# Optimization experiments

Hardware: AMD Instinct MI355X
Metric: run time of the kernel (lower is better)

The kernel has to match this reference:

```python
import jax, jax.numpy as jnp
import numpy as np


def conv(x, w, b):
    # NCHW input, OIHW kernel, stride 1, SAME padding (matches pad=k//2 in torch)
    y = jax.lax.conv_general_dilated(x, w, (1, 1), 'SAME',
                                     dimension_numbers=('NCHW', 'OIHW', 'NCHW'))
    return y + b[None, :, None, None]


def maxpool2(x):
    return jax.lax.reduce_window(x, -jnp.inf, jax.lax.max, (1, 1, 2, 2), (1, 1, 2, 2), 'VALID')


def up(x, s):
    n, c, h, w = x.shape
    # PyTorch nn.Upsample(bilinear, align_corners=False) == half-pixel bilinear
    return jax.image.resize(x, (n, c, h * s, w * s), 'bilinear')


def lin_scan(a, u, axis):
    # h_t = a_t * h_{t-1} + (1 - a_t) * u_t, h_{-1} = 0, via parallel associative scan
    def comb(p, q):
        a1, b1 = p
        a2, b2 = q
        return a1 * a2, a2 * b1 + b2
    return jax.lax.associative_scan(comb, (a, (1.0 - a) * u), axis=axis)[1]


_W_SPECS = [('w_s1', (3, 3, 3, 3)), ('w_mc', (16, 12, 3, 3)), ('w2', (16, 3, 5, 5)),
            ('w3', (32, 16, 3, 3)), ('w4', (32, 32, 3, 3)), ('w5', (32, 32, 3, 3)),
            ('w6', (64, 32, 3, 3)), ('w6s', (64, 64, 3, 3)), ('w7', (32, 96, 3, 3)),
            ('w8', (16, 64, 3, 3)), ('w9', (64, 32, 3, 3)), ('w10', (64, 16, 3, 3)),
            ('w11', (3, 64, 3, 3))]


def setup_inputs():
    key = jax.random.key(0)
    ks = jax.random.split(key, 32)
    inp = {'x': jax.random.normal(ks[0], (2, 3, 512, 512), jnp.float32)}
    for i, (name, sh) in enumerate(_W_SPECS):
        inp[name] = jax.random.normal(ks[i + 1], sh, jnp.float32) * 0.1
        inp['b' + name[1:]] = jax.random.normal(ks[i + 16], (sh[0],), jnp.float32) * 0.01
    return inp


def _forward(x, w_s1, b_s1, w_mc, b_mc, w2, b2, w3, b3, w4, b4, w5, b5, w6, b6,
             w6s, b6s, w7, b7, w8, b8, w9, b9, w10, b10, w11, b11):
    relu = jax.nn.relu
    # multiscale feature input for the spatial RNN
    s1 = conv(x, w_s1, b_s1)
    s2 = maxpool2(s1)
    s3 = maxpool2(s2)
    s4 = maxpool2(s3)
    multi = jnp.concatenate([s1, up(s2, 2), up(s3, 4), up(s4, 8)], axis=1)  # [N,12,H,W]
    ms = conv(multi, w_mc, b_mc)  # [N,16,H,W]
    # gate-prediction encoder/decoder
    c2 = relu(conv(x, w2, b2))                 # [N,16,H,W]
    c3 = relu(conv(maxpool2(c2), w3, b3))      # [N,32,H/2]
    c4 = relu(conv(maxpool2(c3), w4, b4))      # [N,32,H/4]
    c5 = relu(conv(maxpool2(c4), w5, b5))      # [N,32,H/8]
    c6 = relu(conv(maxpool2(c5), w6, b6))      # [N,64,H/16]
    c6re = up(relu(conv(up(c6, 2), w6s, b6s)), 2)               # [N,64,H/4]
    c7 = up(relu(conv(jnp.concatenate([c6re, c4], 1), w7, b7)), 2)  # [N,32,H/2]
    c8 = up(relu(conv(jnp.concatenate([c7, c3], 1), w8, b8)), 2)    # [N,16,H]
    c9 = jnp.tanh(conv(jnp.concatenate([c8, c2], 1), w9, b9))       # [N,64,H,W]
    gx1, gy1, gx2, gy2 = c9[:, 0:16], c9[:, 16:32], c9[:, 32:48], c9[:, 48:64]
    # source quirk: vertical first-pass loops gate with gx1 for steps i>=1 but gy1 row-0 at init
    gate_v = jnp.concatenate([gy1[:, :, 0:1, :], gx1[:, :, 1:, :]], axis=2)
    # first pass: 4-directional gated linear scans over the multiscale features
    h1 = lin_scan(gx1, ms, axis=3)                     # left->right
    h2 = lin_scan(gx1, ms[:, :, :, ::-1], axis=3)      # right->left (stored in scan order)
    h3 = lin_scan(gate_v, ms, axis=2)                  # top->bottom
    h4 = lin_scan(gate_v, ms[:, :, ::-1, :], axis=2)   # bottom->top (stored in scan order)
    # second pass
    h5 = lin_scan(gx2, h1, axis=3)
    h6 = lin_scan(gx2, h2[:, :, :, ::-1], axis=3)
    h7 = lin_scan(gy2, h3, axis=2)
    h8 = lin_scan(gy2, h4[:, :, ::-1, :], axis=2)
    elt_max = jnp.maximum(jnp.maximum(h5, h6), jnp.maximum(h7, h8))
    c10 = relu(conv(elt_max, w10, b10))
    return relu(conv(c10, w11, b11))


def reference(x, w_s1, b_s1, w_mc, b_mc, w2, b2, w3, b3, w4, b4, w5, b5, w6, b6,
              w6s, b6s, w7, b7, w8, b8, w9, b9, w10, b10, w11, b11):
    return _forward(x, w_s1, b_s1, w_mc, b_mc, w2, b2, w3, b3, w4, b4, w5, b5,
                    w6, b6, w6s, b6s, w7, b7, w8, b8, w9, b9, w10, b10, w11, b11)
```

## Files before the change

### kernel.cpp

```cpp
#include <hip/hip_runtime.h>
#include <math.h>

typedef float  f32x4  __attribute__((ext_vector_type(4)));
typedef short  bf16x8 __attribute__((ext_vector_type(8)));

__device__ __forceinline__ ushort f2bf(float f) {
    unsigned u = __float_as_uint(f);
    unsigned r = (u + 0x7fffu + ((u >> 16) & 1u)) >> 16;
    return (ushort)r;
}
__device__ __forceinline__ float bf2f(ushort u) {
    return __uint_as_float(((unsigned)u) << 16);
}
__device__ __forceinline__ float fast_tanh(float x) {
    float e = __expf(2.f * x);
    return 1.f - 2.f / (e + 1.f);
}

__global__ __launch_bounds__(256) void packw_k(
    const float* __restrict__ w, ushort* __restrict__ dst,
    int OCpad, int OCreal, int Cin, int nkb)
{
    int i = blockIdx.x * 256 + threadIdx.x;
    int total = nkb * 9 * OCpad * 32;
    if (i >= total) return;
    int ic32 = i & 31;
    int oc = (i >> 5) % OCpad;
    int t  = (i / (32 * OCpad)) % 9;
    int kb = i / (32 * OCpad * 9);
    int gic = kb * 32 + ic32;
    float v = 0.f;
    if (oc < OCreal && gic < Cin) v = w[((size_t)oc * Cin + gic) * 9 + t];
    dst[i] = f2bf(v);
}

template<int OCB, int NKB, int ACT, int OUTMODE>
__global__ __launch_bounds__(256, 3) void gconv_k(
    const ushort* __restrict__ s0, int n0,
    const ushort* __restrict__ s1, int n1,
    const ushort* __restrict__ Wp, const float* __restrict__ bias,
    void* __restrict__ outp, int H, int W)
{
    constexpr int NB = OCB / 16;
    const int n  = blockIdx.z;
    const int x0 = blockIdx.x * 16, y0 = blockIdx.y * 8;
    const int tid = threadIdx.x;
    const int wid = tid >> 6, lane = tid & 63;
    const int lm = lane & 15, kg = lane >> 4, k0 = kg * 8;
    const bool edge = (x0 == 0) || (x0 + 16 >= W) || (y0 == 0) || (y0 + 8 >= H);
    const int ntot = n0 + n1;
    const size_t HW = (size_t)H * W;

    const ushort* bptr[NKB];
    int bstr[NKB];
    bool bpad[NKB];
#pragma unroll
    for (int kb = 0; kb < NKB; kb++) {
        int gch = kb * 32 + k0;
        if (gch < n0)        { bptr[kb] = s0 + HW * (size_t)(n * n0) + gch;        bstr[kb] = n0; bpad[kb] = false; }
        else if (gch < ntot) { bptr[kb] = s1 + HW * (size_t)(n * n1) + (gch - n0); bstr[kb] = n1; bpad[kb] = false; }
        else                 { bptr[kb] = s0; bstr[kb] = 0; bpad[kb] = true; }
    }

    f32x4 acc[2][NB];
#pragma unroll
    for (int a = 0; a < 2; a++)
#pragma unroll
        for (int b = 0; b < NB; b++) acc[a][b] = (f32x4){0.f, 0.f, 0.f, 0.f};

#pragma unroll
    for (int kb = 0; kb < NKB; kb++) {
        bf16x8 areg[2][9];
#pragma unroll
        for (int ky = 0; ky < 3; ky++)
#pragma unroll
        for (int kx = 0; kx < 3; kx++) {
            const int t = ky * 3 + kx;
#pragma unroll
            for (int mt = 0; mt < 2; mt++) {
                int row = y0 + 2 * wid + mt + ky - 1;
                int xl  = x0 + lm + kx - 1;
                bf16x8 z = (bf16x8){0,0,0,0,0,0,0,0};
                if (!bpad[kb] && (!edge || (row >= 0 && row < H && xl >= 0 && xl < W)))
                    z = *(const bf16x8*)&bptr[kb][((size_t)(row * W + xl)) * bstr[kb]];
                areg[mt][t] = z;
            }
        }
#pragma unroll
        for (int t = 0; t < 9; t++) {
            bf16x8 wf[NB];
#pragma unroll
            for (int nb = 0; nb < NB; nb++)
                wf[nb] = *(const bf16x8*)&Wp[(((kb * 9) + t) * OCB + nb * 16 + lm) * 32 + k0];
#pragma unroll
            for (int nb = 0; nb < NB; nb++) {
#pragma unroll
                for (int mt = 0; mt < 2; mt++)
                    acc[mt][nb] = __builtin_amdgcn_mfma_f32_16x16x32_bf16(areg[mt][t], wf[nb], acc[mt][nb], 0, 0, 0);
            }
        }
    }

    if constexpr (OUTMODE == 0) {
        float* outf = (float*)outp;
#pragma unroll
        for (int mt = 0; mt < 2; mt++) {
            int y = y0 + 2 * wid + mt;
            int x = x0 + kg * 4;
#pragma unroll
            for (int nb = 0; nb < NB; nb++) {
                int oc = nb * 16 + lm;
                float bv = bias[oc];
                float r0 = acc[mt][nb][0] + bv, r1 = acc[mt][nb][1] + bv;
                float r2 = acc[mt][nb][2] + bv, r3 = acc[mt][nb][3] + bv;
                if (ACT == 1) { r0=fmaxf(r0,0.f); r1=fmaxf(r1,0.f); r2=fmaxf(r2,0.f); r3=fmaxf(r3,0.f); }
                if (ACT == 2) { r0=fast_tanh(r0); r1=fast_tanh(r1); r2=fast_tanh(r2); r3=fast_tanh(r3); }
                float4 o; o.x=r0; o.y=r1; o.z=r2; o.w=r3;
                *(float4*)&outf[(((size_t)n * OCB + oc) * H + y) * W + x] = o;
            }
        }
    } else {
        ushort* outb = (ushort*)outp;
        __shared__ ushort Ls[8 * 16 * OCB];
#pragma unroll
        for (int mt = 0; mt < 2; mt++) {
            int yy = 2 * wid + mt;
#pragma unroll
            for (int nb = 0; nb < NB; nb++) {
                int oc = nb * 16 + lm;
                float bv = bias[oc];
#pragma unroll
                for (int r = 0; r < 4; r++) {
                    float v = acc[mt][nb][r] + bv;
                    if (ACT == 1) v = fmaxf(v, 0.f);
                    if (ACT == 2) v = fast_tanh(v);
                    Ls[(yy * 16 + kg * 4 + r) * OCB + oc] = f2bf(v);
                }
            }
        }
        __syncthreads();
#pragma unroll
        for (int q = 0; q < NB; q++) {
            int off = tid * (NB * 8) + q * 8;
            int p = off / OCB, wv = off % OCB;
            int yy = p >> 4, xx = p & 15;
            *(bf16x8*)&outb[((size_t)((n * H + y0 + yy)) * W + x0 + xx) * OCB + wv] =
                *(const bf16x8*)&Ls[off];
        }
    }
}

__global__ __launch_bounds__(256, 3) void gconv11_k(
    const ushort* __restrict__ A, const ushort* __restrict__ Wp,
    const float* __restrict__ bias, float* __restrict__ out)
{
    const int n  = blockIdx.z;
    const int x0 = blockIdx.x * 16, y0 = blockIdx.y * 8;
    const int tid = threadIdx.x;
    const int wid = tid >> 6, lane = tid & 63;
    const int lm = lane & 15, kg = lane >> 4, k0 = kg * 8;
    const bool edge = (x0 == 0) || (x0 == 496) || (y0 == 0) || (y0 == 504);
    const size_t nbase = (size_t)n * 262144 * 64;

    f32x4 acc[2];
    acc[0] = (f32x4){0.f,0.f,0.f,0.f};
    acc[1] = (f32x4){0.f,0.f,0.f,0.f};

#pragma unroll
    for (int kb = 0; kb < 2; kb++) {
        bf16x8 areg[2][9];
#pragma unroll
        for (int ky = 0; ky < 3; ky++)
#pragma unroll
        for (int kx = 0; kx < 3; kx++) {
            const int t = ky * 3 + kx;
#pragma unroll
            for (int mt = 0; mt < 2; mt++) {
                int row = y0 + 2 * wid + mt + ky - 1;
                int xl  = x0 + lm + kx - 1;
                bf16x8 z = (bf16x8){0,0,0,0,0,0,0,0};
                if (!edge || (row >= 0 && row < 512 && xl >= 0 && xl < 512))
                    z = *(const bf16x8*)&A[nbase + ((size_t)(row * 512 + xl)) * 64 + kb * 32 + k0];
                areg[mt][t] = z;
            }
        }
#pragma unroll
        for (int t = 0; t < 9; t++) {
            bf16x8 bfr = *(const bf16x8*)&Wp[((kb * 9 + t) * 16 + lm) * 32 + k0];
#pragma unroll
            for (int mt = 0; mt < 2; mt++)
                acc[mt] = __builtin_amdgcn_mfma_f32_16x16x32_bf16(areg[mt][t], bfr, acc[mt], 0, 0, 0);
        }
    }

    if (lm < 3) {
        float bv = bias[lm];
#pragma unroll
        for (int mt = 0; mt < 2; mt++) {
            int y = y0 + 2 * wid + mt;
            int x = x0 + kg * 4;
            float4 o;
            o.x = fmaxf(acc[mt][0] + bv, 0.f);
            o.y = fmaxf(acc[mt][1] + bv, 0.f);
            o.z = fmaxf(acc[mt][2] + bv, 0.f);
            o.w = fmaxf(acc[mt][3] + bv, 0.f);
            *(float4*)&out[(((size_t)n * 3 + lm) * 512 + y) * 512 + x] = o;
        }
    }
}

__global__ __launch_bounds__(256) void pool_nhwc_k(
    const ushort* __restrict__ in, ushort* __restrict__ out, int C8, int Ho, int Wo)
{
    int idx = blockIdx.x * 256 + threadIdx.x;
    int total = 2 * Ho * Wo * C8;
    if (idx >= total) return;
    int s = idx % C8; int pix = idx / C8;
    int x = pix % Wo; int t = pix / Wo; int y = t % Ho; int n = t / Ho;
    int C = C8 * 8;
    const ushort* p = in + ((size_t)((n * 2 * Ho + 2 * y) * (2 * Wo) + 2 * x)) * C + s * 8;
    bf16x8 a = *(const bf16x8*)p;
    bf16x8 b = *(const bf16x8*)(p + C);
    bf16x8 c = *(const bf16x8*)(p + (size_t)(2 * Wo) * C);
    bf16x8 d = *(const bf16x8*)(p + (size_t)(2 * Wo) * C + C);
    ushort r[8];
#pragma unroll
    for (int j = 0; j < 8; j++) {
        float m = fmaxf(fmaxf(bf2f((ushort)a[j]), bf2f((ushort)b[j])),
                        fmaxf(bf2f((ushort)c[j]), bf2f((ushort)d[j])));
        r[j] = f2bf(m);
    }
    *(bf16x8*)&out[(size_t)pix * C + s * 8] = *(bf16x8*)r;
}

__global__ __launch_bounds__(256) void up_nhwc_k(
    const ushort* __restrict__ in, ushort* __restrict__ out, int C8, int Hi, int Wi)
{
    int Ho = Hi * 2, Wo = Wi * 2;
    int idx = blockIdx.x * 256 + threadIdx.x;
    int total = 2 * Ho * Wo * C8;
    if (idx >= total) return;
    int s = idx % C8; int pix = idx / C8;
    int x = pix % Wo; int t = pix / Wo; int y = t % Ho; int n = t / Ho;
    int C = C8 * 8;
    float sx = (x + 0.5f) * 0.5f - 0.5f;
    float sy = (y + 0.5f) * 0.5f - 0.5f;
    int ix0 = (int)floorf(sx), iy0 = (int)floorf(sy);
    float fx = sx - ix0, fy = sy - iy0;
    int ix1 = ix0 + 1, iy1 = iy0 + 1;
    ix0 = ix0 < 0 ? 0 : ix0;           iy0 = iy0 < 0 ? 0 : iy0;
    ix1 = ix1 > Wi - 1 ? Wi - 1 : ix1; iy1 = iy1 > Hi - 1 ? Hi - 1 : iy1;
    const ushort* base = in + (size_t)n * Hi * Wi * C + s * 8;
    bf16x8 v00 = *(const bf16x8*)&base[((size_t)iy0 * Wi + ix0) * C];
    bf16x8 v01 = *(const bf16x8*)&base[((size_t)iy0 * Wi + ix1) * C];
    bf16x8 v10 = *(const bf16x8*)&base[((size_t)iy1 * Wi + ix0) * C];
    bf16x8 v11 = *(const bf16x8*)&base[((size_t)iy1 * Wi + ix1) * C];
    ushort r[8];
#pragma unroll
    for (int j = 0; j < 8; j++) {
        float a = bf2f((ushort)v00[j]), b = bf2f((ushort)v01[j]);
        float c = bf2f((ushort)v10[j]), d = bf2f((ushort)v11[j]);
        float top = a + fx * (b - a);
        float bot = c + fx * (d - c);
        r[j] = f2bf(top + fy * (bot - top));
    }
    *(bf16x8*)&out[(size_t)pix * C + s * 8] = *(bf16x8*)r;
}

__global__ __launch_bounds__(256) void cvt16_k(
    const float* __restrict__ src, ushort* __restrict__ dst)
{
    int idx = blockIdx.x * 256 + threadIdx.x;
    int x = idx & 511, y = (idx >> 9) & 511, n = idx >> 18;
    const float* base = src + (size_t)n * 16 * 262144 + y * 512 + x;
    ushort vals[16];
#pragma unroll
    for (int c = 0; c < 16; c++) vals[c] = f2bf(base[(size_t)c * 262144]);
    ushort* d = dst + (size_t)idx * 16;
    *(bf16x8*)(d)     = *(bf16x8*)(vals);
    *(bf16x8*)(d + 8) = *(bf16x8*)(vals + 8);
}

template<int K, int OCB, int ACT, int PIX, int OUTW>
__global__ __launch_bounds__(256, 3) void conv_k(
    const float* __restrict__ src0, int c0,
    const float* __restrict__ src1, int c1,
    const float* __restrict__ src2, int c2,
    const float* __restrict__ src3, int c3,
    const float* __restrict__ w, const float* __restrict__ bias,
    void* __restrict__ outp, int H, int W, int OC, int ocChunks)
{
    constexpr int TW = 32, TH = 8 * PIX, P = K / 2;
    constexpr int TLW = TW + K - 1, TLH = TH + K - 1;
    constexpr int TLWP = (K == 3) ? 36 : 40;
    constexpr int CB = 4;
    __shared__ float tile[CB][TLH][TLWP];

    const int z   = blockIdx.z;
    const int n   = z / ocChunks;
    const int ocb = (z - n * ocChunks) * OCB;
    const int tx  = threadIdx.x & 31;
    const int ty  = threadIdx.x >> 5;
    const int x0  = blockIdx.x * TW, y0 = blockIdx.y * TH;
    const int Cin = c0 + c1 + c2 + c3;

    float acc[OCB][PIX];
#pragma unroll
    for (int i = 0; i < OCB; i++)
#pragma unroll
        for (int p = 0; p < PIX; p++) acc[i][p] = 0.f;

    int cgbase = 0;
#pragma unroll
    for (int s = 0; s < 4; s++) {
        const float* sp = (s == 0) ? src0 : (s == 1) ? src1 : (s == 2) ? src2 : src3;
        const int    cn = (s == 0) ? c0   : (s == 1) ? c1   : (s == 2) ? c2   : c3;
        for (int cb = 0; cb < cn; cb += CB) {
            const int nch = (cn - cb < CB) ? (cn - cb) : CB;
            __syncthreads();
            for (int idx = threadIdx.x; idx < nch * TLH * TLW; idx += 256) {
                int ch = idx / (TLH * TLW); int rem = idx - ch * (TLH * TLW);
                int r = rem / TLW, cc = rem - r * TLW;
                int gy = y0 + r - P, gx = x0 + cc - P;
                float vv = 0.f;
                if (gy >= 0 && gy < H && gx >= 0 && gx < W)
                    vv = sp[(size_t)(n * cn + cb + ch) * H * W + (size_t)gy * W + gx];
                tile[ch][r][cc] = vv;
            }
            __syncthreads();
            for (int c = 0; c < nch; c++) {
                float v[PIX + K - 1][K];
#pragma unroll
                for (int r = 0; r < PIX + K - 1; r++)
#pragma unroll
                    for (int cc = 0; cc < K; cc++)
                        v[r][cc] = tile[c][ty * PIX + r][tx + cc];
                const float* wc = w + ((size_t)ocb * Cin + (cgbase + cb + c)) * (K * K);
#pragma unroll
                for (int oc = 0; oc < OCB; oc++) {
                    const float* wo = wc + (size_t)oc * Cin * (K * K);
#pragma unroll
                    for (int ky = 0; ky < K; ky++)
#pragma unroll
                        for (int kx = 0; kx < K; kx++) {
                            float ww = wo[ky * K + kx];
#pragma unroll
                            for (int p = 0; p < PIX; p++)
                                acc[oc][p] = fmaf(ww, v[ky + p][kx], acc[oc][p]);
                        }
                }
            }
        }
        cgbase += cn;
    }

    const int xx = x0 + tx, yy = y0 + ty * PIX;
    if constexpr (OUTW == 0) {
        float* out = (float*)outp;
#pragma unroll
        for (int oc = 0; oc < OCB; oc++) {
            int o = ocb + oc;
            float b = bias[o];
#pragma unroll
            for (int p = 0; p < PIX; p++) {
                float r = acc[oc][p] + b;
                if (ACT == 1) r = fmaxf(r, 0.f);
                if (ACT == 2) r = tanhf(r);
                out[(((size_t)n * OC + o) * H + (yy + p)) * W + xx] = r;
            }
        }
    } else {
        ushort* ob = (ushort*)outp;
#pragma unroll
        for (int p = 0; p < PIX; p++) {
            ushort v16[16];
#pragma unroll
            for (int oc = 0; oc < OCB; oc++) {
                float r = acc[oc][p] + bias[oc];
                if (ACT == 1) r = fmaxf(r, 0.f);
                if (ACT == 2) r = tanhf(r);
                v16[oc] = f2bf(r);
            }
            ushort* d = &ob[(((size_t)n * H + (yy + p)) * W + xx) * 16];
            *(bf16x8*)d       = *(bf16x8*)v16;
            *(bf16x8*)(d + 8) = *(bf16x8*)(v16 + 8);
        }
    }
}

__global__ __launch_bounds__(256) void pool_k(
    const float* __restrict__ in, float* __restrict__ out, int NC, int H, int W)
{
    int H2 = H >> 1, W2 = W >> 1;
    int total = NC * H2 * W2;
    int idx = blockIdx.x * 256 + threadIdx.x;
    if (idx >= total) return;
    int x = idx % W2; int t = idx / W2; int y = t % H2; int q = t / H2;
    const float* p = in + ((size_t)q * H + 2 * y) * W + 2 * x;
    out[idx] = fmaxf(fmaxf(p[0], p[1]), fmaxf(p[W], p[W + 1]));
}

__global__ __launch_bounds__(256) void up_k(
    const float* __restrict__ in, float* __restrict__ out, int NC, int Hi, int Wi, int s)
{
    int Ho = Hi * s, Wo = Wi * s;
    int total = NC * Ho * Wo;
    int idx = blockIdx.x * 256 + threadIdx.x;
    if (idx >= total) return;
    int x = idx % Wo; int t = idx / Wo; int y = t % Ho; int q = t / Ho;
    float inv = 1.0f / (float)s;
    float sx = (x + 0.5f) * inv - 0.5f;
    float sy = (y + 0.5f) * inv - 0.5f;
    int ix0 = (int)floorf(sx), iy0 = (int)floorf(sy);
    float fx = sx - ix0, fy = sy - iy0;
    int ix1 = ix0 + 1, iy1 = iy0 + 1;
    ix0 = ix0 < 0 ? 0 : ix0;           iy0 = iy0 < 0 ? 0 : iy0;
    ix1 = ix1 > Wi - 1 ? Wi - 1 : ix1; iy1 = iy1 > Hi - 1 ? Hi - 1 : iy1;
    const float* p = in + (size_t)q * Hi * Wi;
    float v00 = p[(size_t)iy0 * Wi + ix0], v01 = p[(size_t)iy0 * Wi + ix1];
    float v10 = p[(size_t)iy1 * Wi + ix0], v11 = p[(size_t)iy1 * Wi + ix1];
    float top = v00 + fx * (v01 - v00);
    float bot = v10 + fx * (v11 - v10);
    out[idx] = top + fy * (bot - top);
}

__device__ __forceinline__ void scan_pair(const float a[8], float x1[8], float x2[8], int lane)
{
    float P = 1.f, Q1 = 0.f, Q2 = 0.f;
#pragma unroll
    for (int j = 0; j < 8; j++) {
        float av = a[j];
        Q1 = fmaf(av, Q1, (1.f - av) * x1[j]);
        Q2 = fmaf(av, Q2, (1.f - av) * x2[j]);
        P *= av;
    }
#pragma unroll
    for (int d = 1; d < 64; d <<= 1) {
        float Pp  = __shfl_up(P,  (unsigned)d);
        float Q1p = __shfl_up(Q1, (unsigned)d);
        float Q2p = __shfl_up(Q2, (unsigned)d);
        if (lane >= d) {
            Q1 = fmaf(P, Q1p, Q1);
            Q2 = fmaf(P, Q2p, Q2);
            P *= Pp;
        }
    }
    float h1in = __shfl_up(Q1, 1u);
    float h2in = __shfl_up(Q2, 1u);
    if (lane == 0) { h1in = 0.f; h2in = 0.f; }
    float s1 = h1in, s2 = h2in;
#pragma unroll
    for (int j = 0; j < 8; j++) {
        float av = a[j];
        s1 = fmaf(av, s1, (1.f - av) * x1[j]);
        s2 = fmaf(av, s2, (1.f - av) * x2[j]);
        x1[j] = s1; x2[j] = s2;
    }
}

__global__ __launch_bounds__(256) void scan_h_fused(
    const float* __restrict__ c9, const float* __restrict__ ms,
    float* __restrict__ hm)
{
    int gw   = (blockIdx.x * 256 + threadIdx.x) >> 6;
    int lane = threadIdx.x & 63;
    int y = gw & 511; int nc = gw >> 9; int c = nc & 15; int n = nc >> 4;
    const float* a1row = c9 + ((((size_t)n * 64 + c)      * 512 + y) << 9);
    const float* a2row = c9 + ((((size_t)n * 64 + 32 + c) * 512 + y) << 9);
    const size_t rowoff = (size_t)gw << 9;
    const float* ur = ms + rowoff;
    int t0 = lane << 3;

    float a1[8], a2[8], x1[8], x2[8];
    {
        float4 b0 = *(const float4*)(a1row + t0);
        float4 b1 = *(const float4*)(a1row + t0 + 4);
        a1[0]=b0.x; a1[1]=b0.y; a1[2]=b0.z; a1[3]=b0.w;
        a1[4]=b1.x; a1[5]=b1.y; a1[6]=b1.z; a1[7]=b1.w;
    }
    {
        float4 b0 = *(const float4*)(a2row + t0);
        float4 b1 = *(const float4*)(a2row + t0 + 4);
        a2[0]=b0.x; a2[1]=b0.y; a2[2]=b0.z; a2[3]=b0.w;
        a2[4]=b1.x; a2[5]=b1.y; a2[6]=b1.z; a2[7]=b1.w;
    }
    {
        float4 b0 = *(const float4*)(ur + t0);
        float4 b1 = *(const float4*)(ur + t0 + 4);
        x1[0]=b0.x; x1[1]=b0.y; x1[2]=b0.z; x1[3]=b0.w;
        x1[4]=b1.x; x1[5]=b1.y; x1[6]=b1.z; x1[7]=b1.w;
    }
    {
        float4 r0 = *(const float4*)(ur + (508 - t0));
        float4 r1 = *(const float4*)(ur + (504 - t0));
        x2[0]=r0.w; x2[1]=r0.z; x2[2]=r0.y; x2[3]=r0.x;
        x2[4]=r1.w; x2[5]=r1.z; x2[6]=r1.y; x2[7]=r1.x;
    }

    scan_pair(a1, x1, x2, lane);

    float r[8];
#pragma unroll
    for (int j = 0; j < 8; j++) r[j] = __shfl(x2[7 - j], 63 - lane);

    scan_pair(a2, x1, r, lane);

    float w0[4], w1[4];
#pragma unroll
    for (int j = 0; j < 4; j++) { w0[j] = fmaxf(x1[j], r[j]); w1[j] = fmaxf(x1[j+4], r[j+4]); }
    *(float4*)(hm + rowoff + t0)     = make_float4(w0[0], w0[1], w0[2], w0[3]);
    *(float4*)(hm + rowoff + t0 + 4) = make_float4(w1[0], w1[1], w1[2], w1[3]);
}

#define SV_DECODE \
    int g = blockIdx.x * 256 + threadIdx.x; \
    int x = g & 511; int nc = (g >> 9) & 31; int seg = g >> 14; \
    int c = nc & 15; int n = nc >> 4; int ys = seg << 6; (void)c; (void)n;

__global__ __launch_bounds__(256) void sv_a(
    const float* __restrict__ c9, const float* __restrict__ ms, float* __restrict__ SB)
{
    SV_DECODE
    const float* gx1 = c9 + (((size_t)n * 64 + c)      << 18) + x;
    const float* gy1 = c9 + (((size_t)n * 64 + 16 + c) << 18) + x;
    const float* u   = ms + ((size_t)nc << 18) + x;
    float P = 1.f, Q3 = 0.f, Q4 = 0.f;
    for (int i = 0; i < 64; i++) {
        int y = ys + i;
        float g3 = (y == 0) ? gy1[0] : gx1[(size_t)y << 9];
        float uf = u[(size_t)y << 9];
        float ub = u[(size_t)(511 - y) << 9];
        Q3 = fmaf(g3, Q3, (1.f - g3) * uf);
        Q4 = fmaf(g3, Q4, (1.f - g3) * ub);
        P *= g3;
    }
    SB[g] = P; SB[131072 + g] = Q3; SB[262144 + g] = Q4;
}

__global__ __launch_bounds__(256) void sv_b(
    float* __restrict__ c9, const float* __restrict__ ms,
    float* __restrict__ SB, float* __restrict__ h3buf)
{
    SV_DECODE
    const float* gx1 = c9 + (((size_t)n * 64 + c)      << 18) + x;
    const float* gy1 = c9 + (((size_t)n * 64 + 16 + c) << 18) + x;
    const float* gy2 = c9 + (((size_t)n * 64 + 48 + c) << 18) + x;
    float*       h4p = c9 + (((size_t)n * 64 + 32 + c) << 18) + x;
    const float* u   = ms + ((size_t)nc << 18) + x;
    float*       h3p = h3buf + ((size_t)nc << 18) + x;
    int gc = g & 16383;
    float s3 = 0.f, s4 = 0.f;
    for (int j = 0; j < seg; j++) {
        float Pj  = SB[j * 16384 + gc];
        float Q3j = SB[131072 + j * 16384 + gc];
        float Q4j = SB[262144 + j * 16384 + gc];
        s3 = fmaf(Pj, s3, Q3j);
        s4 = fmaf(Pj, s4, Q4j);
    }
    float P7 = 1.f, Q7 = 0.f;
    for (int i = 0; i < 64; i++) {
        int y = ys + i;
        float g3 = (y == 0) ? gy1[0] : gx1[(size_t)y << 9];
        float uf = u[(size_t)y << 9];
        float ub = u[(size_t)(511 - y) << 9];
        s3 = fmaf(g3, s3, (1.f - g3) * uf);
        s4 = fmaf(g3, s4, (1.f - g3) * ub);
        h3p[(size_t)y << 9] = s3;
        h4p[(size_t)y << 9] = s4;
        float g7 = gy2[(size_t)y << 9];
        Q7 = fmaf(g7, Q7, (1.f - g7) * s3);
        P7 *= g7;
    }
    SB[393216 + g] = P7; SB[524288 + g] = Q7;
}

__global__ __launch_bounds__(256) void sv_c(
    const float* __restrict__ c9, const float* __restrict__ h3buf,
    float* __restrict__ SB, float* __restrict__ hm)
{
    SV_DECODE
    const float* gy2 = c9 + (((size_t)n * 64 + 48 + c) << 18) + x;
    const float* h4p = c9 + (((size_t)n * 64 + 32 + c) << 18) + x;
    const float* h3p = h3buf + ((size_t)nc << 18) + x;
    float*       o   = hm + ((size_t)nc << 18) + x;
    int gc = g & 16383;
    float s7 = 0.f;
    for (int j = 0; j < seg; j++) {
        float Pj = SB[393216 + j * 16384 + gc];
        float Qj = SB[524288 + j * 16384 + gc];
        s7 = fmaf(Pj, s7, Qj);
    }
    float P8 = 1.f, Q8 = 0.f;
    for (int i = 0; i < 64; i++) {
        int y = ys + i;
        float g7 = gy2[(size_t)y << 9];
        float hv = h3p[(size_t)y << 9];
        s7 = fmaf(g7, s7, (1.f - g7) * hv);
        o[(size_t)y << 9] = fmaxf(o[(size_t)y << 9], s7);
        float u8 = h4p[(size_t)(511 - y) << 9];
        Q8 = fmaf(g7, Q8, (1.f - g7) * u8);
        P8 *= g7;
    }
    SB[655360 + g] = P8; SB[786432 + g] = Q8;
}

__global__ __launch_bounds__(256) void sv_d(
    const float* __restrict__ c9, const float* __restrict__ SB, float* __restrict__ hm)
{
    SV_DECODE
    const float* gy2 = c9 + (((size_t)n * 64 + 48 + c) << 18) + x;
    const float* h4p = c9 + (((size_t)n * 64 + 32 + c) << 18) + x;
    float*       o   = hm + ((size_t)nc << 18) + x;
    int gc = g & 16383;
    float s8 = 0.f;
    for (int j = 0; j < seg; j++) {
        float Pj = SB[655360 + j * 16384 + gc];
        float Qj = SB[786432 + j * 16384 + gc];
        s8 = fmaf(Pj, s8, Qj);
    }
    for (int i = 0; i < 64; i++) {
        int y = ys + i;
        float g7 = gy2[(size_t)y << 9];
        float u8 = h4p[(size_t)(511 - y) << 9];
        s8 = fmaf(g7, s8, (1.f - g7) * u8);
        o[(size_t)y << 9] = fmaxf(o[(size_t)y << 9], s8);
    }
}

extern "C" void kernel_launch(void* const* d_in, const int* in_sizes, int n_in,
                              void* d_out, int out_size, void* d_ws, size_t ws_size,
                              hipStream_t stream)
{
    const float* x    = (const float*)d_in[0];
    const float* w_s1 = (const float*)d_in[1];  const float* b_s1 = (const float*)d_in[2];
    const float* w_mc = (const float*)d_in[3];  const float* b_mc = (const float*)d_in[4];
    const float* w2   = (const float*)d_in[5];  const float* b2   = (const float*)d_in[6];
    const float* w3   = (const float*)d_in[7];  const float* b3   = (const float*)d_in[8];
    const float* w4   = (const float*)d_in[9];  const float* b4   = (const float*)d_in[10];
    const float* w5   = (const float*)d_in[11]; const float* b5   = (const float*)d_in[12];
    const float* w6   = (const float*)d_in[13]; const float* b6   = (const float*)d_in[14];
    const float* w6s  = (const float*)d_in[15]; const float* b6s  = (const float*)d_in[16];
    const float* w7   = (const float*)d_in[17]; const float* b7   = (const float*)d_in[18];
    const float* w8   = (const float*)d_in[19]; const float* b8   = (const float*)d_in[20];
    const float* w9   = (const float*)d_in[21]; const float* b9   = (const float*)d_in[22];
    const float* w10  = (const float*)d_in[23]; const float* b10  = (const float*)d_in[24];
    const float* w11  = (const float*)d_in[25]; const float* b11  = (const float*)d_in[26];
    float* out = (float*)d_out;
    float* ws  = (float*)d_ws;

    const size_t NEEDED = 60817408ull * 4ull;
    if (ws_size < NEEDED) return;

    float* MS    = ws;
    float* C9    = ws + 8388608;
    float* H3REG = ws + 41943040;
    float* AR    = ws + 50331648;

    ushort* WREG = (ushort*)AR;
    ushort* wp3  = WREG + 0;      ushort* wp4  = WREG + 9216;
    ushort* wp5  = WREG + 18432;  ushort* wp6  = WREG + 27648;
    ushort* wp6s = WREG + 46080;  ushort* wp7  = WREG + 82944;
    ushort* wp8  = WREG + 110592; ushort* wp9  = WREG + 119808;
    ushort* wp10 = WREG + 138240; ushort* wp11 = WREG + 156672;

    ushort* C2b = (ushort*)(AR + 163840);
    float* s1f = AR + 4358144;
    float* s2f = AR + 5931008;
    float* s3f = AR + 6324224;
    float* s4f = AR + 6422528;
    float* u2  = H3REG + 0;
    float* u3  = H3REG + 1572864;
    float* u4  = H3REG + 3145728;
    ushort* p2    = (ushort*)(AR + 4358144);
    ushort* c3    = (ushort*)(AR + 5406720);
    ushort* p3    = (ushort*)(AR + 7503872);
    ushort* c4    = (ushort*)(AR + 8028160);
    ushort* p4    = (ushort*)(AR + 8552448);
    ushort* c5    = (ushort*)(AR + 8683520);
    ushort* p5    = (ushort*)(AR + 8814592);
    ushort* c6    = (ushort*)(AR + 8847360);
    ushort* u6    = (ushort*)(AR + 8912896);
    ushort* t6    = (ushort*)(AR + 9175040);
    ushort* c6re  = (ushort*)(AR + 9437184);
    ushort* c7pre = (ushort*)(AR + 7503872);
    ushort* c7    = (ushort*)(AR + 8028160);
    ushort* c8pre = (ushort*)(AR + 4358144);
    ushort* c8b   = (ushort*)(AR + 5406720);
    float* SB  = AR + 163840;
    float* HM  = AR + 1081344;
    float* H3  = H3REG;
    ushort* A10 = (ushort*)H3REG;
    ushort* A11 = (ushort*)C9;

    auto cdiv = [](int a, int b) { return (a + b - 1) / b; };

    packw_k<<<36,256,0,stream>>>(w3,  wp3,  32, 32, 16, 1);
    packw_k<<<36,256,0,stream>>>(w4,  wp4,  32, 32, 32, 1);
    packw_k<<<36,256,0,stream>>>(w5,  wp5,  32, 32, 32, 1);
    packw_k<<<72,256,0,stream>>>(w6,  wp6,  64, 64, 32, 1);
    packw_k<<<144,256,0,stream>>>(w6s, wp6s, 64, 64, 64, 2);
    packw_k<<<108,256,0,stream>>>(w7,  wp7,  32, 32, 96, 3);
    packw_k<<<36,256,0,stream>>>(w8,  wp8,  16, 16, 64, 2);
    packw_k<<<72,256,0,stream>>>(w9,  wp9,  64, 64, 32, 1);
    packw_k<<<72,256,0,stream>>>(w10, wp10, 64, 64, 16, 1);
    packw_k<<<36,256,0,stream>>>(w11, wp11, 16, 3,  64, 2);

    conv_k<5,16,1,2,1><<<dim3(16,32,2),256,0,stream>>>(x,3,nullptr,0,nullptr,0,nullptr,0,
                                                       w2,b2, C2b, 512,512,16,1);
    conv_k<3,3,0,2,0><<<dim3(16,32,2),256,0,stream>>>(x,3,nullptr,0,nullptr,0,nullptr,0,
                                                      w_s1,b_s1, s1f, 512,512,3,1);
    pool_k<<<cdiv(2*3*256*256,256),256,0,stream>>>(s1f, s2f, 6, 512, 512);
    pool_k<<<cdiv(2*3*128*128,256),256,0,stream>>>(s2f, s3f, 6, 256, 256);
    pool_k<<<cdiv(2*3*64*64,  256),256,0,stream>>>(s3f, s4f, 6, 128, 128);
    up_k<<<6144,256,0,stream>>>(s2f, u2, 6, 256, 256, 2);
    up_k<<<6144,256,0,stream>>>(s3f, u3, 6, 128, 128, 4);
    up_k<<<6144,256,0,stream>>>(s4f, u4, 6, 64, 64, 8);
    conv_k<3,16,0,2,0><<<dim3(16,32,2),256,0,stream>>>(s1f,3,u2,3,u3,3,u4,3,
                                                       w_mc,b_mc, MS, 512,512,16,1);

    pool_nhwc_k<<<1024,256,0,stream>>>(C2b, p2, 2, 256, 256);
    gconv_k<32,1,1,1><<<dim3(16,32,2),256,0,stream>>>(p2,16,nullptr,0, wp3,b3, c3, 256,256);
    pool_nhwc_k<<<512,256,0,stream>>>(c3, p3, 4, 128, 128);
    gconv_k<32,1,1,1><<<dim3(8,16,2),256,0,stream>>>(p3,32,nullptr,0, wp4,b4, c4, 128,128);
    pool_nhwc_k<<<128,256,0,stream>>>(c4, p4, 4, 64, 64);
    gconv_k<32,1,1,1><<<dim3(4,8,2),256,0,stream>>>(p4,32,nullptr,0, wp5,b5, c5, 64,64);
    pool_nhwc_k<<<32,256,0,stream>>>(c5, p5, 4, 32, 32);
    gconv_k<64,1,1,1><<<dim3(2,4,2),256,0,stream>>>(p5,32,nullptr,0, wp6,b6, c6, 32,32);
    up_nhwc_k<<<256,256,0,stream>>>(c6, u6, 8, 32, 32);
    gconv_k<64,2,1,1><<<dim3(4,8,2),256,0,stream>>>(u6,64,nullptr,0, wp6s,b6s, t6, 64,64);
    up_nhwc_k<<<1024,256,0,stream>>>(t6, c6re, 8, 64, 64);
    gconv_k<32,3,1,1><<<dim3(8,16,2),256,0,stream>>>(c6re,64, c4,32, wp7,b7, c7pre, 128,128);
    up_nhwc_k<<<2048,256,0,stream>>>(c7pre, c7, 4, 128, 128);
    gconv_k<16,2,1,1><<<dim3(16,32,2),256,0,stream>>>(c7,32, c3,32, wp8,b8, c8pre, 256,256);
    up_nhwc_k<<<4096,256,0,stream>>>(c8pre, c8b, 2, 256, 256);
    gconv_k<64,1,2,0><<<dim3(32,64,2),256,0,stream>>>(c8b,16, C2b,16, wp9,b9, C9, 512,512);

    scan_h_fused<<<4096,256,0,stream>>>(C9, MS, HM);
    sv_a<<<512,256,0,stream>>>(C9, MS, SB);
    sv_b<<<512,256,0,stream>>>(C9, MS, SB, H3);
    sv_c<<<512,256,0,stream>>>(C9, H3, SB, HM);
    sv_d<<<512,256,0,stream>>>(C9, SB, HM);

    cvt16_k<<<2048,256,0,stream>>>(HM, A10);
    gconv_k<64,1,1,1><<<dim3(32,64,2),256,0,stream>>>(A10,16,nullptr,0, wp10,b10, A11, 512,512);
    gconv11_k<<<dim3(32,64,2),256,0,stream>>>(A11, wp11, b11, out);
    (void)in_sizes; (void)n_in; (void)out_size; (void)ws_size;
}
```

Before: 670.7 us.

## Tile full-res convs as 16x16 blocks with per-warp 4-row register reuse

Adds new conv kernels where each block covers a 16x16 tile and each warp computes 4 output rows. For each kx column shift a warp loads 6 input rows once and reuses them across the 3 ky taps, where the old code loaded 9 fragments per output row pair. The three 512x512 convolutions (w9, w10, w11) switch to these kernels with half as many blocks. This cuts redundant global and L2 loads of activations, at the cost of more accumulator registers per thread, which may reduce occupancy.

```diff
diff --git a/kernel.cpp b/kernel.cpp
--- a/kernel.cpp
+++ b/kernel.cpp
@@ -35,6 +35,177 @@
 }
 
 template<int OCB, int NKB, int ACT, int OUTMODE>
+__global__ __launch_bounds__(256, 3) void gconv_mr(
+    const ushort* __restrict__ s0, int n0,
+    const ushort* __restrict__ s1, int n1,
+    const ushort* __restrict__ Wp, const float* __restrict__ bias,
+    void* __restrict__ outp, int H, int W)
+{
+    constexpr int NB = OCB / 16;
+    const int n  = blockIdx.z;
+    const int x0 = blockIdx.x * 16, y0 = blockIdx.y * 16;
+    const int tid = threadIdx.x;
+    const int wid = tid >> 6, lane = tid & 63;
+    const int lm = lane & 15, kg = lane >> 4, k0 = kg * 8;
+    const int ry = y0 + 4 * wid;
+    const bool edge = (x0 == 0) || (x0 + 16 >= W) || (ry == 0) || (ry + 4 >= H);
+    const int ntot = n0 + n1;
+    const size_t HW = (size_t)H * W;
+
+    const ushort* bptr[NKB];
+    int bstr[NKB];
+    bool bpad[NKB];
+#pragma unroll
+    for (int kb = 0; kb < NKB; kb++) {
+        int gch = kb * 32 + k0;
+        if (gch < n0)        { bptr[kb] = s0 + HW * (size_t)(n * n0) + gch;        bstr[kb] = n0; bpad[kb] = false; }
+        else if (gch < ntot) { bptr[kb] = s1 + HW * (size_t)(n * n1) + (gch - n0); bstr[kb] = n1; bpad[kb] = false; }
+        else                 { bptr[kb] = s0; bstr[kb] = 0; bpad[kb] = true; }
+    }
+
+    f32x4 acc[4][NB];
+#pragma unroll
+    for (int m = 0; m < 4; m++)
+#pragma unroll
+        for (int b = 0; b < NB; b++) acc[m][b] = (f32x4){0.f, 0.f, 0.f, 0.f};
+
+#pragma unroll
+    for (int kb = 0; kb < NKB; kb++) {
+#pragma unroll
+        for (int kx = 0; kx < 3; kx++) {
+            bf16x8 ar[6];
+            const int xl = x0 + lm + kx - 1;
+#pragma unroll
+            for (int r6 = 0; r6 < 6; r6++) {
+                int row = ry + r6 - 1;
+                bf16x8 z = (bf16x8){0,0,0,0,0,0,0,0};
+                if (!bpad[kb] && (!edge || (row >= 0 && row < H && xl >= 0 && xl < W)))
+                    z = *(const bf16x8*)&bptr[kb][((size_t)(row * W + xl)) * bstr[kb]];
+                ar[r6] = z;
+            }
+#pragma unroll
+            for (int ky = 0; ky < 3; ky++) {
+                bf16x8 wf[NB];
+#pragma unroll
+                for (int nb = 0; nb < NB; nb++)
+                    wf[nb] = *(const bf16x8*)&Wp[(((kb * 9) + ky * 3 + kx) * OCB + nb * 16 + lm) * 32 + k0];
+#pragma unroll
+                for (int nb = 0; nb < NB; nb++)
+#pragma unroll
+                    for (int m = 0; m < 4; m++)
+                        acc[m][nb] = __builtin_amdgcn_mfma_f32_16x16x32_bf16(ar[m + ky], wf[nb], acc[m][nb], 0, 0, 0);
+            }
+        }
+    }
+
+    if constexpr (OUTMODE == 0) {
+        float* outf = (float*)outp;
+#pragma unroll
+        for (int m = 0; m < 4; m++) {
+            int y = ry + m;
+            int x = x0 + kg * 4;
+#pragma unroll
+            for (int nb = 0; nb < NB; nb++) {
+                int oc = nb * 16 + lm;
+                float bv = bias[oc];
+                float r0 = acc[m][nb][0] + bv, r1 = acc[m][nb][1] + bv;
+                float r2 = acc[m][nb][2] + bv, r3 = acc[m][nb][3] + bv;
+                if (ACT == 1) { r0=fmaxf(r0,0.f); r1=fmaxf(r1,0.f); r2=fmaxf(r2,0.f); r3=fmaxf(r3,0.f); }
+                if (ACT == 2) { r0=fast_tanh(r0); r1=fast_tanh(r1); r2=fast_tanh(r2); r3=fast_tanh(r3); }
+                float4 o; o.x=r0; o.y=r1; o.z=r2; o.w=r3;
+                *(float4*)&outf[(((size_t)n * OCB + oc) * H + y) * W + x] = o;
+            }
+        }
+    } else {
+        ushort* outb = (ushort*)outp;
+        __shared__ ushort Ls[16 * 16 * OCB];
+#pragma unroll
+        for (int m = 0; m < 4; m++) {
+            int yy = 4 * wid + m;
+#pragma unroll
+            for (int nb = 0; nb < NB; nb++) {
+                int oc = nb * 16 + lm;
+                float bv = bias[oc];
+#pragma unroll
+                for (int r = 0; r < 4; r++) {
+                    float v = acc[m][nb][r] + bv;
+                    if (ACT == 1) v = fmaxf(v, 0.f);
+                    if (ACT == 2) v = fast_tanh(v);
+                    Ls[(yy * 16 + kg * 4 + r) * OCB + oc] = f2bf(v);
+                }
+            }
+        }
+        __syncthreads();
+        constexpr int NQ = OCB / 8;
+#pragma unroll
+        for (int q = 0; q < NQ; q++) {
+            int off = q * 2048 + tid * 8;
+            int p = off / OCB, wv = off % OCB;
+            int yy = p >> 4, xx = p & 15;
+            *(bf16x8*)&outb[((size_t)((n * H + y0 + yy)) * W + x0 + xx) * OCB + wv] =
+                *(const bf16x8*)&Ls[off];
+        }
+    }
+}
+
+__global__ __launch_bounds__(256, 3) void gconv11_mr(
+    const ushort* __restrict__ A, const ushort* __restrict__ Wp,
+    const float* __restrict__ bias, float* __restrict__ out)
+{
+    const int n  = blockIdx.z;
+    const int x0 = blockIdx.x * 16, y0 = blockIdx.y * 16;
+    const int tid = threadIdx.x;
+    const int wid = tid >> 6, lane = tid & 63;
+    const int lm = lane & 15, kg = lane >> 4, k0 = kg * 8;
+    const int ry = y0 + 4 * wid;
+    const bool edge = (x0 == 0) || (x0 + 16 >= 512) || (ry == 0) || (ry + 4 >= 512);
+    const size_t nbase = (size_t)n * 262144 * 64;
+
+    f32x4 acc[4];
+#pragma unroll
+    for (int m = 0; m < 4; m++) acc[m] = (f32x4){0.f,0.f,0.f,0.f};
+
+#pragma unroll
+    for (int kb = 0; kb < 2; kb++) {
+#pragma unroll
+        for (int kx = 0; kx < 3; kx++) {
+            bf16x8 ar[6];
+            const int xl = x0 + lm + kx - 1;
+#pragma unroll
+            for (int r6 = 0; r6 < 6; r6++) {
+                int row = ry + r6 - 1;
+                bf16x8 z = (bf16x8){0,0,0,0,0,0,0,0};
+                if (!edge || (row >= 0 && row < 512 && xl >= 0 && xl < 512))
+                    z = *(const bf16x8*)&A[nbase + ((size_t)(row * 512 + xl)) * 64 + kb * 32 + k0];
+                ar[r6] = z;
+            }
+#pragma unroll
+            for (int ky = 0; ky < 3; ky++) {
+                bf16x8 wf = *(const bf16x8*)&Wp[((kb * 9 + ky * 3 + kx) * 16 + lm) * 32 + k0];
+#pragma unroll
+                for (int m = 0; m < 4; m++)
+                    acc[m] = __builtin_amdgcn_mfma_f32_16x16x32_bf16(ar[m + ky], wf, acc[m], 0, 0, 0);
+            }
+        }
+    }
+
+    if (lm < 3) {
+        float bv = bias[lm];
+#pragma unroll
+        for (int m = 0; m < 4; m++) {
+            int y = ry + m;
+            int x = x0 + kg * 4;
+            float4 o;
+            o.x = fmaxf(acc[m][0] + bv, 0.f);
+            o.y = fmaxf(acc[m][1] + bv, 0.f);
+            o.z = fmaxf(acc[m][2] + bv, 0.f);
+            o.w = fmaxf(acc[m][3] + bv, 0.f);
+            *(float4*)&out[(((size_t)n * 3 + lm) * 512 + y) * 512 + x] = o;
+        }
+    }
+}
+
+template<int OCB, int NKB, int ACT, int OUTMODE>
 __global__ __launch_bounds__(256, 3) void gconv_k(
     const ushort* __restrict__ s0, int n0,
     const ushort* __restrict__ s1, int n1,
@@ -146,65 +317,6 @@
             int yy = p >> 4, xx = p & 15;
             *(bf16x8*)&outb[((size_t)((n * H + y0 + yy)) * W + x0 + xx) * OCB + wv] =
                 *(const bf16x8*)&Ls[off];
-        }
-    }
-}
-
-__global__ __launch_bounds__(256, 3) void gconv11_k(
-    const ushort* __restrict__ A, const ushort* __restrict__ Wp,
-    const float* __restrict__ bias, float* __restrict__ out)
-{
-    const int n  = blockIdx.z;
-    const int x0 = blockIdx.x * 16, y0 = blockIdx.y * 8;
-    const int tid = threadIdx.x;
-    const int wid = tid >> 6, lane = tid & 63;
-    const int lm = lane & 15, kg = lane >> 4, k0 = kg * 8;
-    const bool edge = (x0 == 0) || (x0 == 496) || (y0 == 0) || (y0 == 504);
-    const size_t nbase = (size_t)n * 262144 * 64;
-
-    f32x4 acc[2];
-    acc[0] = (f32x4){0.f,0.f,0.f,0.f};
-    acc[1] = (f32x4){0.f,0.f,0.f,0.f};
-
-#pragma unroll
-    for (int kb = 0; kb < 2; kb++) {
-        bf16x8 areg[2][9];
-#pragma unroll
-        for (int ky = 0; ky < 3; ky++)
-#pragma unroll
-        for (int kx = 0; kx < 3; kx++) {
-            const int t = ky * 3 + kx;
-#pragma unroll
-            for (int mt = 0; mt < 2; mt++) {
-                int row = y0 + 2 * wid + mt + ky - 1;
-                int xl  = x0 + lm + kx - 1;
-                bf16x8 z = (bf16x8){0,0,0,0,0,0,0,0};
-                if (!edge || (row >= 0 && row < 512 && xl >= 0 && xl < 512))
-                    z = *(const bf16x8*)&A[nbase + ((size_t)(row * 512 + xl)) * 64 + kb * 32 + k0];
-                areg[mt][t] = z;
-            }
-        }
-#pragma unroll
-        for (int t = 0; t < 9; t++) {
-            bf16x8 bfr = *(const bf16x8*)&Wp[((kb * 9 + t) * 16 + lm) * 32 + k0];
-#pragma unroll
-            for (int mt = 0; mt < 2; mt++)
-                acc[mt] = __builtin_amdgcn_mfma_f32_16x16x32_bf16(areg[mt][t], bfr, acc[mt], 0, 0, 0);
-        }
-    }
-
-    if (lm < 3) {
-        float bv = bias[lm];
-#pragma unroll
-        for (int mt = 0; mt < 2; mt++) {
-            int y = y0 + 2 * wid + mt;
-            int x = x0 + kg * 4;
-            float4 o;
-            o.x = fmaxf(acc[mt][0] + bv, 0.f);
-            o.y = fmaxf(acc[mt][1] + bv, 0.f);
-            o.z = fmaxf(acc[mt][2] + bv, 0.f);
-            o.w = fmaxf(acc[mt][3] + bv, 0.f);
-            *(float4*)&out[(((size_t)n * 3 + lm) * 512 + y) * 512 + x] = o;
         }
     }
 }
@@ -733,7 +845,7 @@
     up_nhwc_k<<<2048,256,0,stream>>>(c7pre, c7, 4, 128, 128);
     gconv_k<16,2,1,1><<<dim3(16,32,2),256,0,stream>>>(c7,32, c3,32, wp8,b8, c8pre, 256,256);
     up_nhwc_k<<<4096,256,0,stream>>>(c8pre, c8b, 2, 256, 256);
-    gconv_k<64,1,2,0><<<dim3(32,64,2),256,0,stream>>>(c8b,16, C2b,16, wp9,b9, C9, 512,512);
+    gconv_mr<64,1,2,0><<<dim3(32,32,2),256,0,stream>>>(c8b,16, C2b,16, wp9,b9, C9, 512,512);
 
     scan_h_fused<<<4096,256,0,stream>>>(C9, MS, HM);
     sv_a<<<512,256,0,stream>>>(C9, MS, SB);
@@ -742,7 +854,7 @@
     sv_d<<<512,256,0,stream>>>(C9, SB, HM);
 
     cvt16_k<<<2048,256,0,stream>>>(HM, A10);
-    gconv_k<64,1,1,1><<<dim3(32,64,2),256,0,stream>>>(A10,16,nullptr,0, wp10,b10, A11, 512,512);
-    gconv11_k<<<dim3(32,64,2),256,0,stream>>>(A11, wp11, b11, out);
+    gconv_mr<64,1,1,1><<<dim3(32,32,2),256,0,stream>>>(A10,16,nullptr,0, wp10,b10, A11, 512,512);
+    gconv11_mr<<<dim3(32,32,2),256,0,stream>>>(A11, wp11, b11, out);
     (void)in_sizes; (void)n_in; (void)out_size; (void)ws_size;
 }
```

New measurement: 698.8 us. +4.2%, slower.
